# Kernel optimization log

Hardware: AMD Instinct MI355X
Metric: run time of the kernel (lower is better)

## Reference

```python
import jax, jax.numpy as jnp
import numpy as np

N = 100000      # nodes
E = 1600000     # edges (avg degree 16)
F_IN = 128      # node feature dim
F_E = 8         # edge feature dim
H = 4           # attention heads (layer 1)
C = 16          # hidden per head
T = 1           # target size (layer 2, heads=1, concat=False)
NEG_SLOPE = 0.2


def setup_inputs() -> dict:
    key = jax.random.key(0)
    ks = jax.random.split(key, 20)
    g = lambda k, shape, fan: (jax.random.normal(k, shape, jnp.float32) / np.sqrt(fan))
    return {
        "x": jax.random.normal(ks[0], (N, F_IN), jnp.float32),
        "edge_index": jax.random.randint(ks[1], (2, E), 0, N, dtype=jnp.int32),
        "edge_attr": jax.random.normal(ks[2], (E, F_E), jnp.float32),
        # layer 1 (in=F_IN, out=C, heads=H, concat=True, edge_dim=F_E)
        "Wl1": g(ks[3], (F_IN, H * C), F_IN),
        "bl1": jnp.zeros((H * C,), jnp.float32),
        "Wr1": g(ks[4], (F_IN, H * C), F_IN),
        "br1": jnp.zeros((H * C,), jnp.float32),
        "We1": g(ks[5], (F_E, H * C), F_E),
        "att1": g(ks[6], (H, C), C),
        "b1": jnp.zeros((H * C,), jnp.float32),
        # layer 2 (in=H*C, out=T, heads=1, concat=False, edge_dim=F_E)
        "Wl2": g(ks[7], (H * C, T), H * C),
        "bl2": jnp.zeros((T,), jnp.float32),
        "Wr2": g(ks[8], (H * C, T), H * C),
        "br2": jnp.zeros((T,), jnp.float32),
        "We2": g(ks[9], (F_E, T), F_E),
        "att2": g(ks[10], (1, T), T),
        "b2": jnp.zeros((T,), jnp.float32),
    }


def _gatv2(x, src, dst, eattr, Wl, bl, Wr, br, We, att, bias, heads, out_ch, concat, n_nodes):
    # add self loops, self-loop edge_attr = mean of edge_attr (PyG fill_value='mean')
    loop = jnp.arange(n_nodes, dtype=src.dtype)
    src_a = jnp.concatenate([src, loop])
    dst_a = jnp.concatenate([dst, loop])
    ea = jnp.concatenate(
        [eattr, jnp.broadcast_to(eattr.mean(axis=0), (n_nodes, eattr.shape[1]))], axis=0)

    xl = (x @ Wl + bl).reshape(n_nodes, heads, out_ch)   # source transform
    xr = (x @ Wr + br).reshape(n_nodes, heads, out_ch)   # target transform
    ee = (ea @ We).reshape(-1, heads, out_ch)            # edge transform (no bias)

    # GATv2: score = att . LeakyReLU(x_l[src] + x_r[dst] + W_e e)
    s = jax.nn.leaky_relu(xl[src_a] + xr[dst_a] + ee, NEG_SLOPE)  # [Ea,H,C]
    logits = jnp.einsum('ehc,hc->eh', s, att)                      # [Ea,H]

    # segment softmax over destination nodes (every node has a self loop)
    m = jax.ops.segment_max(logits, dst_a, num_segments=n_nodes)   # [N,H]
    p = jnp.exp(logits - m[dst_a])
    denom = jax.ops.segment_sum(p, dst_a, num_segments=n_nodes)
    alpha = p / denom[dst_a]                                        # [Ea,H]

    out = jax.ops.segment_sum(xl[src_a] * alpha[:, :, None], dst_a,
                              num_segments=n_nodes)                 # [N,H,C]
    out = out.reshape(n_nodes, heads * out_ch) if concat else out.mean(axis=1)
    return out + bias


def reference(x, edge_index, edge_attr, Wl1, bl1, Wr1, br1, We1, att1, b1,
              Wl2, bl2, Wr2, br2, We2, att2, b2):
    src, dst = edge_index[0], edge_index[1]
    # dropout layers are identity at eval time (training=False)
    h = _gatv2(x, src, dst, edge_attr, Wl1, bl1, Wr1, br1, We1, att1, b1,
               H, C, True, N)
    h = jax.nn.elu(h)
    out = _gatv2(h, src, dst, edge_attr, Wl2, bl2, Wr2, br2, We2, att2, b2,
                 1, T, False, N)
    return out
```

## Files before the change

kernel.cpp:

```cpp
#include <hip/hip_runtime.h>
#include <math.h>

#define N_NODES 100000
#define N_EDGES 1600000
#define N_ITEMS (N_EDGES + N_NODES)
#define F_IN 128
#define F_E 8
#define HC 64
#define NHEAD 4
#define NEG 0.2f
#define SCAN_BS 1024
#define SCAN_NB ((N_NODES + SCAN_BS - 1) / SCAN_BS)
#define MS_BLOCKS 1024
#define NEG_BIG (-3.0e38f)

__global__ void init_deg(unsigned* __restrict__ deg) {
    int i = blockIdx.x * blockDim.x + threadIdx.x;
    if (i < N_NODES) deg[i] = 1u;
}

__global__ void mean_sum_kernel(const float* __restrict__ ea, float* __restrict__ partials) {
    __shared__ float sh[4][8];
    float acc[8] = {0.f,0.f,0.f,0.f,0.f,0.f,0.f,0.f};
    int stride = gridDim.x * blockDim.x;
    for (int r = blockIdx.x * blockDim.x + threadIdx.x; r < N_EDGES; r += stride) {
        const float4* p = (const float4*)(ea + (size_t)r * 8);
        float4 a = p[0], b = p[1];
        acc[0] += a.x; acc[1] += a.y; acc[2] += a.z; acc[3] += a.w;
        acc[4] += b.x; acc[5] += b.y; acc[6] += b.z; acc[7] += b.w;
    }
    int wid  = threadIdx.x >> 6;
    int lane = threadIdx.x & 63;
#pragma unroll
    for (int k = 0; k < 8; k++) {
        float v = acc[k];
        for (int off = 32; off; off >>= 1) v += __shfl_down(v, off);
        if (lane == 0) sh[wid][k] = v;
    }
    __syncthreads();
    if (threadIdx.x < 8) {
        float s = sh[0][threadIdx.x] + sh[1][threadIdx.x] + sh[2][threadIdx.x] + sh[3][threadIdx.x];
        partials[blockIdx.x * 8 + threadIdx.x] = s;
    }
}

__global__ void reduce_sum8(const float* __restrict__ partials, float* __restrict__ sum8) {
    int lane = threadIdx.x;
    int c = lane & 7, g = lane >> 3;
    float s = 0.f;
    for (int b = g; b < MS_BLOCKS; b += 8) s += partials[b * 8 + c];
    s += __shfl_xor(s, 8);
    s += __shfl_xor(s, 16);
    s += __shfl_xor(s, 32);
    if (lane < 8) sum8[lane] = s;
}

__global__ void hist_kernel(const int* __restrict__ dst, unsigned* __restrict__ deg) {
    int e = blockIdx.x * blockDim.x + threadIdx.x;
    if (e < N_EDGES) atomicAdd(&deg[dst[e]], 1u);
}

__global__ void scan1(const unsigned* __restrict__ deg, unsigned* __restrict__ local_inc,
                      unsigned* __restrict__ bsum) {
    __shared__ unsigned tmp[SCAN_BS];
    int i = blockIdx.x * SCAN_BS + threadIdx.x;
    unsigned v = (i < N_NODES) ? deg[i] : 0u;
    tmp[threadIdx.x] = v;
    __syncthreads();
    for (int off = 1; off < SCAN_BS; off <<= 1) {
        unsigned add = (threadIdx.x >= (unsigned)off) ? tmp[threadIdx.x - off] : 0u;
        __syncthreads();
        tmp[threadIdx.x] += add;
        __syncthreads();
    }
    if (i < N_NODES) local_inc[i] = tmp[threadIdx.x];
    if (threadIdx.x == SCAN_BS - 1) bsum[blockIdx.x] = tmp[threadIdx.x];
}

__global__ void scan2(unsigned* __restrict__ bsum) {
    __shared__ unsigned tmp[128];
    int t = threadIdx.x;
    unsigned v = (t < SCAN_NB) ? bsum[t] : 0u;
    tmp[t] = v;
    __syncthreads();
    for (int off = 1; off < 128; off <<= 1) {
        unsigned add = (t >= off) ? tmp[t - off] : 0u;
        __syncthreads();
        tmp[t] += add;
        __syncthreads();
    }
    if (t < SCAN_NB) bsum[t] = tmp[t] - v;
}

__global__ void scan3(const unsigned* __restrict__ local_inc, const unsigned* __restrict__ deg,
                      const unsigned* __restrict__ bsum,
                      unsigned* __restrict__ row_start, unsigned* __restrict__ next) {
    int i = blockIdx.x * blockDim.x + threadIdx.x;
    if (i >= N_NODES) return;
    unsigned v = local_inc[i] - deg[i] + bsum[i / SCAN_BS];
    row_start[i] = v;
    next[i] = v;
}

__global__ void scatter_kernel(const int* __restrict__ src, const int* __restrict__ dst,
                               const float* __restrict__ ea, const float* __restrict__ sum8,
                               unsigned* __restrict__ next,
                               int* __restrict__ sorted_src, float* __restrict__ sorted_ea) {
    int item = blockIdx.x * blockDim.x + threadIdx.x;
    if (item >= N_ITEMS) return;
    int s, d;
    float4 a, b;
    if (item < N_EDGES) {
        s = src[item]; d = dst[item];
        const float4* p = (const float4*)(ea + (size_t)item * 8);
        a = p[0]; b = p[1];
    } else {
        s = d = item - N_EDGES;
        const float inv = 1.0f / N_EDGES;
        a = make_float4(sum8[0]*inv, sum8[1]*inv, sum8[2]*inv, sum8[3]*inv);
        b = make_float4(sum8[4]*inv, sum8[5]*inv, sum8[6]*inv, sum8[7]*inv);
    }
    unsigned pos = atomicAdd(&next[d], 1u);
    sorted_src[pos] = s;
    float4* q = (float4*)(sorted_ea + (size_t)pos * 8);
    q[0] = a; q[1] = b;
}

__global__ __launch_bounds__(256) void gemm1_kernel(
        const float* __restrict__ x,
        const float* __restrict__ Wl, const float* __restrict__ bl,
        const float* __restrict__ Wr, const float* __restrict__ br,
        float* __restrict__ xl, float* __restrict__ xr) {
    __shared__ float xs_t[F_IN][36];
    int t = threadIdx.x & 31;
    int g = threadIdx.x >> 5;
    const float* Wsel = (t < 16) ? Wl : Wr;
    const float* bsel = (t < 16) ? bl : br;
    int jc = (t < 16) ? 4 * t : 4 * t - HC;
    float4 bias = *(const float4*)(bsel + jc);
    float* dstp = (t < 16) ? xl : xr;

    int n0 = blockIdx.x * 32;
    int row = threadIdx.x >> 3;
    int cq  = threadIdx.x & 7;
#pragma unroll
    for (int r = 0; r < 4; r++) {
        int c = cq * 4 + r * 32;
        float4 v = *(const float4*)(x + (size_t)(n0 + row) * F_IN + c);
        xs_t[c + 0][row] = v.x;
        xs_t[c + 1][row] = v.y;
        xs_t[c + 2][row] = v.z;
        xs_t[c + 3][row] = v.w;
    }
    __syncthreads();
    int nb = g * 4;
    float4 a0 = bias, a1 = bias, a2 = bias, a3 = bias;
#pragma unroll 4
    for (int k = 0; k < F_IN; k++) {
        float4 w  = *(const float4*)(Wsel + k * HC + jc);
        float4 xv = *(const float4*)&xs_t[k][nb];
        a0.x += w.x * xv.x; a0.y += w.y * xv.x; a0.z += w.z * xv.x; a0.w += w.w * xv.x;
        a1.x += w.x * xv.y; a1.y += w.y * xv.y; a1.z += w.z * xv.y; a1.w += w.w * xv.y;
        a2.x += w.x * xv.z; a2.y += w.y * xv.z; a2.z += w.z * xv.z; a2.w += w.w * xv.z;
        a3.x += w.x * xv.w; a3.y += w.y * xv.w; a3.z += w.z * xv.w; a3.w += w.w * xv.w;
    }
    *(float4*)(dstp + (size_t)(n0 + nb + 0) * HC + jc) = a0;
    *(float4*)(dstp + (size_t)(n0 + nb + 1) * HC + jc) = a1;
    *(float4*)(dstp + (size_t)(n0 + nb + 2) * HC + jc) = a2;
    *(float4*)(dstp + (size_t)(n0 + nb + 3) * HC + jc) = a3;
}

__global__ void gat1_kernel(const unsigned* __restrict__ row_start, const unsigned* __restrict__ deg,
                            const int* __restrict__ ssrc, const float* __restrict__ sea,
                            const float* __restrict__ We1, const float* __restrict__ att1,
                            const float* __restrict__ b1,
                            const float* __restrict__ xl, const float* __restrict__ xr,
                            const float* __restrict__ Wl2, const float* __restrict__ bl2,
                            const float* __restrict__ Wr2, const float* __restrict__ br2,
                            float* __restrict__ xl2, float* __restrict__ xr2) {
    int node = blockIdx.x * (blockDim.x >> 6) + (threadIdx.x >> 6);
    int lane = threadIdx.x & 63;
    if (node >= N_NODES) return;
    int g  = lane >> 4;
    int cl = lane & 15;
    unsigned start = row_start[node];
    unsigned cnt   = deg[node];

    float4 we[8];
#pragma unroll
    for (int k = 0; k < 8; k++) we[k] = *(const float4*)(We1 + k * HC + 4 * cl);
    float4 attv = *(const float4*)(att1 + 4 * cl);
    float4 xrv  = *(const float4*)(xr + (size_t)node * HC + 4 * cl);

    float m = NEG_BIG, den = 0.f;
    float4 acc = make_float4(0.f, 0.f, 0.f, 0.f);

    bool valid_n = ((unsigned)g < cnt);
    unsigned safe = valid_n ? start + g : start;
    int s_n = ssrc[safe];
    float4 ea0_n = *(const float4*)(sea + (size_t)safe * 8);
    float4 ea1_n = *(const float4*)(sea + (size_t)safe * 8 + 4);
    float4 xl_n  = *(const float4*)(xl + (size_t)s_n * HC + 4 * cl);

    for (unsigned j = 0; j < cnt; j += 4) {
        bool valid = valid_n;
        float4 ea0 = ea0_n, ea1 = ea1_n, xlv = xl_n;
        unsigned jn = j + 4;
        if (jn < cnt) {
            valid_n = (jn + g < cnt);
            unsigned sf = valid_n ? start + jn + g : start;
            s_n = ssrc[sf];
            ea0_n = *(const float4*)(sea + (size_t)sf * 8);
            ea1_n = *(const float4*)(sea + (size_t)sf * 8 + 4);
            xl_n  = *(const float4*)(xl + (size_t)s_n * HC + 4 * cl);
        }
        float4 v;
        v.x = xlv.x + xrv.x + ea0.x*we[0].x + ea0.y*we[1].x + ea0.z*we[2].x + ea0.w*we[3].x
                            + ea1.x*we[4].x + ea1.y*we[5].x + ea1.z*we[6].x + ea1.w*we[7].x;
        v.y = xlv.y + xrv.y + ea0.x*we[0].y + ea0.y*we[1].y + ea0.z*we[2].y + ea0.w*we[3].y
                            + ea1.x*we[4].y + ea1.y*we[5].y + ea1.z*we[6].y + ea1.w*we[7].y;
        v.z = xlv.z + xrv.z + ea0.x*we[0].z + ea0.y*we[1].z + ea0.z*we[2].z + ea0.w*we[3].z
                            + ea1.x*we[4].z + ea1.y*we[5].z + ea1.z*we[6].z + ea1.w*we[7].z;
        v.w = xlv.w + xrv.w + ea0.x*we[0].w + ea0.y*we[1].w + ea0.z*we[2].w + ea0.w*we[3].w
                            + ea1.x*we[4].w + ea1.y*we[5].w + ea1.z*we[6].w + ea1.w*we[7].w;
        v.x = v.x > 0.f ? v.x : NEG * v.x;
        v.y = v.y > 0.f ? v.y : NEG * v.y;
        v.z = v.z > 0.f ? v.z : NEG * v.z;
        v.w = v.w > 0.f ? v.w : NEG * v.w;
        float prod = v.x*attv.x + v.y*attv.y + v.z*attv.z + v.w*attv.w;
        prod += __shfl_xor(prod, 1);
        prod += __shfl_xor(prod, 2);
        float logit = valid ? prod : NEG_BIG;
        float mnew  = fmaxf(m, logit);
        float scale = __expf(m - mnew);
        float p     = valid ? __expf(logit - mnew) : 0.f;
        den   = den   * scale + p;
        acc.x = acc.x * scale + p * xlv.x;
        acc.y = acc.y * scale + p * xlv.y;
        acc.z = acc.z * scale + p * xlv.z;
        acc.w = acc.w * scale + p * xlv.w;
        m = mnew;
    }
    float M = m;
    M = fmaxf(M, __shfl_xor(M, 16));
    M = fmaxf(M, __shfl_xor(M, 32));
    float gs = __expf(m - M);
    den *= gs; acc.x *= gs; acc.y *= gs; acc.z *= gs; acc.w *= gs;
    den   += __shfl_xor(den, 16);   den   += __shfl_xor(den, 32);
    acc.x += __shfl_xor(acc.x, 16); acc.x += __shfl_xor(acc.x, 32);
    acc.y += __shfl_xor(acc.y, 16); acc.y += __shfl_xor(acc.y, 32);
    acc.z += __shfl_xor(acc.z, 16); acc.z += __shfl_xor(acc.z, 32);
    acc.w += __shfl_xor(acc.w, 16); acc.w += __shfl_xor(acc.w, 32);

    float4 b1v  = *(const float4*)(b1 + 4 * cl);
    float4 wl2v = *(const float4*)(Wl2 + 4 * cl);
    float4 wr2v = *(const float4*)(Wr2 + 4 * cl);
    float inv_den = 1.f / den;
    float4 o;
    o.x = acc.x * inv_den + b1v.x;
    o.y = acc.y * inv_den + b1v.y;
    o.z = acc.z * inv_den + b1v.z;
    o.w = acc.w * inv_den + b1v.w;
    o.x = o.x > 0.f ? o.x : expm1f(o.x);
    o.y = o.y > 0.f ? o.y : expm1f(o.y);
    o.z = o.z > 0.f ? o.z : expm1f(o.z);
    o.w = o.w > 0.f ? o.w : expm1f(o.w);
    float sl = o.x*wl2v.x + o.y*wl2v.y + o.z*wl2v.z + o.w*wl2v.w;
    float sr = o.x*wr2v.x + o.y*wr2v.y + o.z*wr2v.z + o.w*wr2v.w;
#pragma unroll
    for (int off = 1; off <= 8; off <<= 1) {
        sl += __shfl_xor(sl, off);
        sr += __shfl_xor(sr, off);
    }
    if (lane == 0) {
        xl2[node] = sl + bl2[0];
        xr2[node] = sr + br2[0];
    }
}

__global__ void gat2_kernel(const unsigned* __restrict__ row_start, const unsigned* __restrict__ deg,
                            const int* __restrict__ sorted_src, const float* __restrict__ sorted_ea,
                            const float* __restrict__ We2, const float* __restrict__ att2,
                            const float* __restrict__ xl2, const float* __restrict__ xr2,
                            const float* __restrict__ b2, float* __restrict__ out) {
    int node = blockIdx.x * (blockDim.x >> 6) + (threadIdx.x >> 6);
    int lane = threadIdx.x & 63;
    if (node >= N_NODES) return;
    unsigned start = row_start[node];
    unsigned cnt   = deg[node];
    float xrv = xr2[node];
    float a2  = att2[0];
    float m = -INFINITY, den = 0.f, num = 0.f;
    for (unsigned base = 0; base < cnt; base += 64) {
        unsigned idx = base + lane;
        float logit = -INFINITY, xv = 0.f;
        if (idx < cnt) {
            int s = sorted_src[start + idx];
            const float* eap = sorted_ea + (size_t)(start + idx) * 8;
            float ee = 0.f;
#pragma unroll
            for (int k = 0; k < 8; k++) ee += eap[k] * We2[k];
            xv = xl2[s];
            float v = xv + xrv + ee;
            v = v > 0.f ? v : NEG * v;
            logit = a2 * v;
        }
        float mm = logit;
        for (int off = 1; off < 64; off <<= 1) mm = fmaxf(mm, __shfl_xor(mm, off));
        float mnew = fmaxf(m, mm);
        float p  = (idx < cnt) ? __expf(logit - mnew) : 0.f;
        float pn = p * xv;
        for (int off = 1; off < 64; off <<= 1) {
            p  += __shfl_xor(p, off);
            pn += __shfl_xor(pn, off);
        }
        float scale = __expf(m - mnew);
        den = den * scale + p;
        num = num * scale + pn;
        m = mnew;
    }
    if (lane == 0) out[node] = num / den + b2[0];
}

extern "C" void kernel_launch(void* const* d_in, const int* in_sizes, int n_in,
                              void* d_out, int out_size, void* d_ws, size_t ws_size,
                              hipStream_t stream) {
    const float* x    = (const float*)d_in[0];
    const int*   ei   = (const int*)d_in[1];
    const float* ea   = (const float*)d_in[2];
    const float* Wl1  = (const float*)d_in[3];
    const float* bl1  = (const float*)d_in[4];
    const float* Wr1  = (const float*)d_in[5];
    const float* br1  = (const float*)d_in[6];
    const float* We1  = (const float*)d_in[7];
    const float* att1 = (const float*)d_in[8];
    const float* b1   = (const float*)d_in[9];
    const float* Wl2  = (const float*)d_in[10];
    const float* bl2  = (const float*)d_in[11];
    const float* Wr2  = (const float*)d_in[12];
    const float* br2  = (const float*)d_in[13];
    const float* We2  = (const float*)d_in[14];
    const float* att2 = (const float*)d_in[15];
    const float* b2   = (const float*)d_in[16];

    const int* src = ei;
    const int* dst = ei + N_EDGES;

    float* W = (float*)d_ws;
    size_t o = 0;
    float*    sum8      = W + o;               o += 8;
    float*    partials  = W + o;               o += MS_BLOCKS * 8;
    unsigned* deg       = (unsigned*)(W + o);  o += N_NODES;
    unsigned* local_inc = (unsigned*)(W + o);  o += N_NODES;
    unsigned* bsum      = (unsigned*)(W + o);  o += 128;
    unsigned* row_start = (unsigned*)(W + o);  o += N_NODES;
    unsigned* next      = (unsigned*)(W + o);  o += N_NODES;
    int*      ssrc      = (int*)(W + o);       o += N_ITEMS;
    o = (o + 3) & ~(size_t)3;
    float*    sea       = W + o;               o += (size_t)N_ITEMS * 8;
    float*    xl1       = W + o;               o += (size_t)N_NODES * HC;
    float*    xr1       = W + o;               o += (size_t)N_NODES * HC;
    float*    xl2       = W + o;               o += N_NODES;
    float*    xr2       = W + o;               o += N_NODES;

    init_deg<<<(N_NODES + 255) / 256, 256, 0, stream>>>(deg);
    mean_sum_kernel<<<MS_BLOCKS, 256, 0, stream>>>(ea, partials);
    reduce_sum8<<<1, 64, 0, stream>>>(partials, sum8);
    hist_kernel<<<(N_EDGES + 255) / 256, 256, 0, stream>>>(dst, deg);
    scan1<<<SCAN_NB, SCAN_BS, 0, stream>>>(deg, local_inc, bsum);
    scan2<<<1, 128, 0, stream>>>(bsum);
    scan3<<<(N_NODES + 255) / 256, 256, 0, stream>>>(local_inc, deg, bsum, row_start, next);
    scatter_kernel<<<(N_ITEMS + 255) / 256, 256, 0, stream>>>(src, dst, ea, sum8, next, ssrc, sea);
    gemm1_kernel<<<N_NODES / 32, 256, 0, stream>>>(x, Wl1, bl1, Wr1, br1, xl1, xr1);
    gat1_kernel<<<(N_NODES + 3) / 4, 256, 0, stream>>>(
        row_start, deg, ssrc, sea, We1, att1, b1, xl1, xr1,
        Wl2, bl2, Wr2, br2, xl2, xr2);
    gat2_kernel<<<(N_NODES + 3) / 4, 256, 0, stream>>>(
        row_start, deg, ssrc, sea, We2, att2, xl2, xr2, b2, (float*)d_out);
}
```

Measured before the change: 455.4 us.

## Dual-stream gat1 edge loop, precompute layer-2 edge term, fold deg init

The gat1 per-node edge loop now handles eight edges per iteration in two independent online-softmax streams, each with its own prefetch. The streams are merged at the end, which doubles the memory loads in flight per wave at the cost of more registers. The scatter kernel now computes the layer-2 edge projection (edge_attr·We2) once per edge into a compact array. gat2 therefore reads one float per edge instead of eight. Degree initialisation is folded into the mean-sum kernel, removing one launch.

```diff
diff --git a/kernel.cpp b/kernel.cpp
--- a/kernel.cpp
+++ b/kernel.cpp
@@ -14,15 +14,13 @@
 #define MS_BLOCKS 1024
 #define NEG_BIG (-3.0e38f)
 
-__global__ void init_deg(unsigned* __restrict__ deg) {
-    int i = blockIdx.x * blockDim.x + threadIdx.x;
-    if (i < N_NODES) deg[i] = 1u;
-}
-
-__global__ void mean_sum_kernel(const float* __restrict__ ea, float* __restrict__ partials) {
+__global__ void mean_sum_kernel(const float* __restrict__ ea, float* __restrict__ partials,
+                                unsigned* __restrict__ deg) {
     __shared__ float sh[4][8];
+    int stride = gridDim.x * blockDim.x;
+    for (int i = blockIdx.x * blockDim.x + threadIdx.x; i < N_NODES; i += stride)
+        deg[i] = 1u;
     float acc[8] = {0.f,0.f,0.f,0.f,0.f,0.f,0.f,0.f};
-    int stride = gridDim.x * blockDim.x;
     for (int r = blockIdx.x * blockDim.x + threadIdx.x; r < N_EDGES; r += stride) {
         const float4* p = (const float4*)(ea + (size_t)r * 8);
         float4 a = p[0], b = p[1];
@@ -104,8 +102,10 @@
 
 __global__ void scatter_kernel(const int* __restrict__ src, const int* __restrict__ dst,
                                const float* __restrict__ ea, const float* __restrict__ sum8,
+                               const float* __restrict__ We2,
                                unsigned* __restrict__ next,
-                               int* __restrict__ sorted_src, float* __restrict__ sorted_ea) {
+                               int* __restrict__ sorted_src, float* __restrict__ sorted_ea,
+                               float* __restrict__ see2) {
     int item = blockIdx.x * blockDim.x + threadIdx.x;
     if (item >= N_ITEMS) return;
     int s, d;
@@ -120,8 +120,11 @@
         a = make_float4(sum8[0]*inv, sum8[1]*inv, sum8[2]*inv, sum8[3]*inv);
         b = make_float4(sum8[4]*inv, sum8[5]*inv, sum8[6]*inv, sum8[7]*inv);
     }
+    float ee2 = a.x*We2[0] + a.y*We2[1] + a.z*We2[2] + a.w*We2[3]
+              + b.x*We2[4] + b.y*We2[5] + b.z*We2[6] + b.w*We2[7];
     unsigned pos = atomicAdd(&next[d], 1u);
     sorted_src[pos] = s;
+    see2[pos] = ee2;
     float4* q = (float4*)(sorted_ea + (size_t)pos * 8);
     q[0] = a; q[1] = b;
 }
@@ -168,6 +171,52 @@
     *(float4*)(dstp + (size_t)(n0 + nb + 1) * HC + jc) = a1;
     *(float4*)(dstp + (size_t)(n0 + nb + 2) * HC + jc) = a2;
     *(float4*)(dstp + (size_t)(n0 + nb + 3) * HC + jc) = a3;
+}
+
+__device__ __forceinline__ void load_edge(const int* __restrict__ ssrc,
+                                          const float* __restrict__ sea,
+                                          const float* __restrict__ xl,
+                                          unsigned start, unsigned cnt, unsigned idx, int cl,
+                                          bool& valid, float4& e0, float4& e1, float4& xv) {
+    valid = (idx < cnt);
+    unsigned sf = valid ? start + idx : start;
+    int s = ssrc[sf];
+    e0 = *(const float4*)(sea + (size_t)sf * 8);
+    e1 = *(const float4*)(sea + (size_t)sf * 8 + 4);
+    xv = *(const float4*)(xl + (size_t)s * HC + 4 * cl);
+}
+
+__device__ __forceinline__ void edge_update(const float4* __restrict__ we,
+                                            const float4& attv, const float4& xrv,
+                                            bool valid, const float4& ea0, const float4& ea1,
+                                            const float4& xlv,
+                                            float& m, float& den, float4& acc) {
+    float4 v;
+    v.x = xlv.x + xrv.x + ea0.x*we[0].x + ea0.y*we[1].x + ea0.z*we[2].x + ea0.w*we[3].x
+                        + ea1.x*we[4].x + ea1.y*we[5].x + ea1.z*we[6].x + ea1.w*we[7].x;
+    v.y = xlv.y + xrv.y + ea0.x*we[0].y + ea0.y*we[1].y + ea0.z*we[2].y + ea0.w*we[3].y
+                        + ea1.x*we[4].y + ea1.y*we[5].y + ea1.z*we[6].y + ea1.w*we[7].y;
+    v.z = xlv.z + xrv.z + ea0.x*we[0].z + ea0.y*we[1].z + ea0.z*we[2].z + ea0.w*we[3].z
+                        + ea1.x*we[4].z + ea1.y*we[5].z + ea1.z*we[6].z + ea1.w*we[7].z;
+    v.w = xlv.w + xrv.w + ea0.x*we[0].w + ea0.y*we[1].w + ea0.z*we[2].w + ea0.w*we[3].w
+                        + ea1.x*we[4].w + ea1.y*we[5].w + ea1.z*we[6].w + ea1.w*we[7].w;
+    v.x = v.x > 0.f ? v.x : NEG * v.x;
+    v.y = v.y > 0.f ? v.y : NEG * v.y;
+    v.z = v.z > 0.f ? v.z : NEG * v.z;
+    v.w = v.w > 0.f ? v.w : NEG * v.w;
+    float prod = v.x*attv.x + v.y*attv.y + v.z*attv.z + v.w*attv.w;
+    prod += __shfl_xor(prod, 1);
+    prod += __shfl_xor(prod, 2);
+    float logit = valid ? prod : NEG_BIG;
+    float mnew  = fmaxf(m, logit);
+    float scale = __expf(m - mnew);
+    float p     = valid ? __expf(logit - mnew) : 0.f;
+    den   = den   * scale + p;
+    acc.x = acc.x * scale + p * xlv.x;
+    acc.y = acc.y * scale + p * xlv.y;
+    acc.z = acc.z * scale + p * xlv.z;
+    acc.w = acc.w * scale + p * xlv.w;
+    m = mnew;
 }
 
 __global__ void gat1_kernel(const unsigned* __restrict__ row_start, const unsigned* __restrict__ deg,
@@ -192,55 +241,35 @@
     float4 attv = *(const float4*)(att1 + 4 * cl);
     float4 xrv  = *(const float4*)(xr + (size_t)node * HC + 4 * cl);
 
-    float m = NEG_BIG, den = 0.f;
-    float4 acc = make_float4(0.f, 0.f, 0.f, 0.f);
-
-    bool valid_n = ((unsigned)g < cnt);
-    unsigned safe = valid_n ? start + g : start;
-    int s_n = ssrc[safe];
-    float4 ea0_n = *(const float4*)(sea + (size_t)safe * 8);
-    float4 ea1_n = *(const float4*)(sea + (size_t)safe * 8 + 4);
-    float4 xl_n  = *(const float4*)(xl + (size_t)s_n * HC + 4 * cl);
-
-    for (unsigned j = 0; j < cnt; j += 4) {
-        bool valid = valid_n;
-        float4 ea0 = ea0_n, ea1 = ea1_n, xlv = xl_n;
-        unsigned jn = j + 4;
+    float mA = NEG_BIG, denA = 0.f, mB = NEG_BIG, denB = 0.f;
+    float4 accA = make_float4(0.f,0.f,0.f,0.f), accB = make_float4(0.f,0.f,0.f,0.f);
+
+    bool vA_n, vB_n;
+    float4 e0A_n, e1A_n, xA_n, e0B_n, e1B_n, xB_n;
+    load_edge(ssrc, sea, xl, start, cnt, g,     cl, vA_n, e0A_n, e1A_n, xA_n);
+    load_edge(ssrc, sea, xl, start, cnt, 4 + g, cl, vB_n, e0B_n, e1B_n, xB_n);
+
+    for (unsigned j = 0; j < cnt; j += 8) {
+        bool vA = vA_n, vB = vB_n;
+        float4 e0A = e0A_n, e1A = e1A_n, xA = xA_n;
+        float4 e0B = e0B_n, e1B = e1B_n, xB = xB_n;
+        unsigned jn = j + 8;
         if (jn < cnt) {
-            valid_n = (jn + g < cnt);
-            unsigned sf = valid_n ? start + jn + g : start;
-            s_n = ssrc[sf];
-            ea0_n = *(const float4*)(sea + (size_t)sf * 8);
-            ea1_n = *(const float4*)(sea + (size_t)sf * 8 + 4);
-            xl_n  = *(const float4*)(xl + (size_t)s_n * HC + 4 * cl);
+            load_edge(ssrc, sea, xl, start, cnt, jn + g,     cl, vA_n, e0A_n, e1A_n, xA_n);
+            load_edge(ssrc, sea, xl, start, cnt, jn + 4 + g, cl, vB_n, e0B_n, e1B_n, xB_n);
         }
-        float4 v;
-        v.x = xlv.x + xrv.x + ea0.x*we[0].x + ea0.y*we[1].x + ea0.z*we[2].x + ea0.w*we[3].x
-                            + ea1.x*we[4].x + ea1.y*we[5].x + ea1.z*we[6].x + ea1.w*we[7].x;
-        v.y = xlv.y + xrv.y + ea0.x*we[0].y + ea0.y*we[1].y + ea0.z*we[2].y + ea0.w*we[3].y
-                            + ea1.x*we[4].y + ea1.y*we[5].y + ea1.z*we[6].y + ea1.w*we[7].y;
-        v.z = xlv.z + xrv.z + ea0.x*we[0].z + ea0.y*we[1].z + ea0.z*we[2].z + ea0.w*we[3].z
-                            + ea1.x*we[4].z + ea1.y*we[5].z + ea1.z*we[6].z + ea1.w*we[7].z;
-        v.w = xlv.w + xrv.w + ea0.x*we[0].w + ea0.y*we[1].w + ea0.z*we[2].w + ea0.w*we[3].w
-                            + ea1.x*we[4].w + ea1.y*we[5].w + ea1.z*we[6].w + ea1.w*we[7].w;
-        v.x = v.x > 0.f ? v.x : NEG * v.x;
-        v.y = v.y > 0.f ? v.y : NEG * v.y;
-        v.z = v.z > 0.f ? v.z : NEG * v.z;
-        v.w = v.w > 0.f ? v.w : NEG * v.w;
-        float prod = v.x*attv.x + v.y*attv.y + v.z*attv.z + v.w*attv.w;
-        prod += __shfl_xor(prod, 1);
-        prod += __shfl_xor(prod, 2);
-        float logit = valid ? prod : NEG_BIG;
-        float mnew  = fmaxf(m, logit);
-        float scale = __expf(m - mnew);
-        float p     = valid ? __expf(logit - mnew) : 0.f;
-        den   = den   * scale + p;
-        acc.x = acc.x * scale + p * xlv.x;
-        acc.y = acc.y * scale + p * xlv.y;
-        acc.z = acc.z * scale + p * xlv.z;
-        acc.w = acc.w * scale + p * xlv.w;
-        m = mnew;
-    }
+        edge_update(we, attv, xrv, vA, e0A, e1A, xA, mA, denA, accA);
+        edge_update(we, attv, xrv, vB, e0B, e1B, xB, mB, denB, accB);
+    }
+    float m = fmaxf(mA, mB);
+    float sA = __expf(mA - m), sB = __expf(mB - m);
+    float den = denA * sA + denB * sB;
+    float4 acc;
+    acc.x = accA.x * sA + accB.x * sB;
+    acc.y = accA.y * sA + accB.y * sB;
+    acc.z = accA.z * sA + accB.z * sB;
+    acc.w = accA.w * sA + accB.w * sB;
+
     float M = m;
     M = fmaxf(M, __shfl_xor(M, 16));
     M = fmaxf(M, __shfl_xor(M, 32));
@@ -279,8 +308,8 @@
 }
 
 __global__ void gat2_kernel(const unsigned* __restrict__ row_start, const unsigned* __restrict__ deg,
-                            const int* __restrict__ sorted_src, const float* __restrict__ sorted_ea,
-                            const float* __restrict__ We2, const float* __restrict__ att2,
+                            const int* __restrict__ sorted_src, const float* __restrict__ see2,
+                            const float* __restrict__ att2,
                             const float* __restrict__ xl2, const float* __restrict__ xr2,
                             const float* __restrict__ b2, float* __restrict__ out) {
     int node = blockIdx.x * (blockDim.x >> 6) + (threadIdx.x >> 6);
@@ -296,10 +325,7 @@
         float logit = -INFINITY, xv = 0.f;
         if (idx < cnt) {
             int s = sorted_src[start + idx];
-            const float* eap = sorted_ea + (size_t)(start + idx) * 8;
-            float ee = 0.f;
-#pragma unroll
-            for (int k = 0; k < 8; k++) ee += eap[k] * We2[k];
+            float ee = see2[start + idx];
             xv = xl2[s];
             float v = xv + xrv + ee;
             v = v > 0.f ? v : NEG * v;
@@ -356,6 +382,7 @@
     unsigned* row_start = (unsigned*)(W + o);  o += N_NODES;
     unsigned* next      = (unsigned*)(W + o);  o += N_NODES;
     int*      ssrc      = (int*)(W + o);       o += N_ITEMS;
+    float*    see2      = W + o;               o += N_ITEMS;
     o = (o + 3) & ~(size_t)3;
     float*    sea       = W + o;               o += (size_t)N_ITEMS * 8;
     float*    xl1       = W + o;               o += (size_t)N_NODES * HC;
@@ -363,18 +390,18 @@
     float*    xl2       = W + o;               o += N_NODES;
     float*    xr2       = W + o;               o += N_NODES;
 
-    init_deg<<<(N_NODES + 255) / 256, 256, 0, stream>>>(deg);
-    mean_sum_kernel<<<MS_BLOCKS, 256, 0, stream>>>(ea, partials);
+    mean_sum_kernel<<<MS_BLOCKS, 256, 0, stream>>>(ea, partials, deg);
     reduce_sum8<<<1, 64, 0, stream>>>(partials, sum8);
     hist_kernel<<<(N_EDGES + 255) / 256, 256, 0, stream>>>(dst, deg);
     scan1<<<SCAN_NB, SCAN_BS, 0, stream>>>(deg, local_inc, bsum);
     scan2<<<1, 128, 0, stream>>>(bsum);
     scan3<<<(N_NODES + 255) / 256, 256, 0, stream>>>(local_inc, deg, bsum, row_start, next);
-    scatter_kernel<<<(N_ITEMS + 255) / 256, 256, 0, stream>>>(src, dst, ea, sum8, next, ssrc, sea);
+    scatter_kernel<<<(N_ITEMS + 255) / 256, 256, 0, stream>>>(
+        src, dst, ea, sum8, We2, next, ssrc, sea, see2);
     gemm1_kernel<<<N_NODES / 32, 256, 0, stream>>>(x, Wl1, bl1, Wr1, br1, xl1, xr1);
     gat1_kernel<<<(N_NODES + 3) / 4, 256, 0, stream>>>(
         row_start, deg, ssrc, sea, We1, att1, b1, xl1, xr1,
         Wl2, bl2, Wr2, br2, xl2, xr2);
     gat2_kernel<<<(N_NODES + 3) / 4, 256, 0, stream>>>(
-        row_start, deg, ssrc, sea, We2, att2, xl2, xr2, b2, (float*)d_out);
-}
+        row_start, deg, ssrc, see2, att2, xl2, xr2, b2, (float*)d_out);
+}
```

Result: faster. 435.3 us (median of 2 runs) (-4.4%).
